# Kernel optimization log

Hardware: AMD Instinct MI355X
Metric: run time of the kernel (lower is better)

Reference implementation:

```python
import jax, jax.numpy as jnp
import numpy as np

B, C, H, W = 4096, 1, 64, 64
NCLASS = 10
ALPHA = 1.0
EPS = 1e-8  # torch CosineSimilarity eps


def setup_inputs() -> dict:
    key = jax.random.key(0)
    k1, k2, k3 = jax.random.split(key, 3)
    outputs = jax.random.normal(k1, (B, NCLASS), dtype=jnp.float32)
    grad = jax.random.normal(k2, (B, C, H, W), dtype=jnp.float32)
    y = jax.random.randint(k3, (B,), 0, NCLASS)
    return {"outputs": outputs, "grad": grad, "y": y}


def reference(outputs, grad, y):
    b = grad.shape[0]
    # per-sample min-max normalization over all of (C,H,W)
    flat = grad.reshape(b, -1)                      # [B, C*H*W]
    gmax = flat.max(axis=1, keepdims=True)
    gmin = flat.min(axis=1, keepdims=True)
    ngrad = (flat - gmin) / (gmax - gmin)           # [B, D]

    # batched pairwise cosine similarity: normalize + matmul
    norms = jnp.linalg.norm(ngrad, axis=1, keepdims=True)
    vn = ngrad / jnp.maximum(norms, EPS)
    sim = vn @ vn.T                                 # [B, B]

    # pairs (i<j) with the same predicted class (argmax(softmax(o)) == argmax(o))
    pred = jnp.argmax(outputs, axis=1)
    same = pred[:, None] == pred[None, :]
    upper = jnp.triu(jnp.ones((b, b), dtype=bool), k=1)
    mask = same & upper
    xloss = jnp.sum(jnp.where(mask, 1.0 - sim, 0.0)) / b

    # cross-entropy
    logp = jax.nn.log_softmax(outputs, axis=1)
    celoss = -jnp.take_along_axis(logp, y[:, None], axis=1).sum() / b
    return celoss + ALPHA * xloss
```

## Files before the change

kernel.cpp:

```cpp
#include <hip/hip_runtime.h>
#include <math.h>

constexpr int Dn = 4096;
constexpr int Bn = 4096;
constexpr int NCLS = 10;

constexpr int OFF_CUR   = 0;
constexpr int OFF_CE    = 10;
constexpr int OFF_XS    = 11;
constexpr int OFF_NCH   = 12;
constexpr int OFF_CHS   = 16;
constexpr int OFF_A     = 32;
constexpr int OFF_B2    = 4128;
constexpr int OFF_ORD   = 8224;
constexpr int OFF_CHMAP = 49184;
constexpr int OFF_P     = 49456;

__global__ __launch_bounds__(256) void pass0_ce_order(
    const float* __restrict__ outputs, const int* __restrict__ y,
    float* __restrict__ ws)
{
    const int t = threadIdx.x;
    const int i = blockIdx.x * 256 + t;
    const int wave = t >> 6, lane = t & 63;
    int* wsi = (int*)ws;

    __shared__ int hist[NCLS];
    __shared__ int lbase[NCLS];
    __shared__ float sce[4];
    if (t < NCLS) hist[t] = 0;
    __syncthreads();

    const float* o = outputs + (size_t)i * NCLS;
    float m = o[0]; int am = 0;
    #pragma unroll
    for (int k = 1; k < NCLS; ++k) { float ok = o[k]; if (ok > m) { m = ok; am = k; } }
    float se = 0.f;
    #pragma unroll
    for (int k = 0; k < NCLS; ++k) se += expf(o[k] - m);
    float ce = m + logf(se) - o[y[i]];

    int rank = atomicAdd(&hist[am], 1);

    #pragma unroll
    for (int off = 32; off; off >>= 1) ce += __shfl_down(ce, off, 64);
    if (lane == 0) sce[wave] = ce;
    __syncthreads();

    if (t < NCLS) lbase[t] = atomicAdd(&wsi[OFF_CUR + t], hist[t]);
    if (t == 0) atomicAdd(&ws[OFF_CE], sce[0] + sce[1] + sce[2] + sce[3]);
    __syncthreads();

    wsi[OFF_ORD + am * Bn + lbase[am] + rank] = i;
}

__global__ void sched_chunks(float* __restrict__ ws, int CH)
{
    int* wsi = (int*)ws;
    int nch = 0;
    for (int c = 0; c < NCLS; ++c) {
        wsi[OFF_CHS + c] = nch;
        int n = wsi[OFF_CUR + c];
        for (int s = 0; s < n; s += CH)
            wsi[OFF_CHMAP + nch++] = (c << 16) | s;
    }
    wsi[OFF_CHS + NCLS] = nch;
    wsi[OFF_NCH] = nch;
}

__global__ __launch_bounds__(256) void pass1_stats(
    const float* __restrict__ grad, float* __restrict__ ws)
{
    const int i = blockIdx.x;
    const int t = threadIdx.x;
    const int wave = t >> 6, lane = t & 63;

    const float4* g4 = (const float4*)(grad + (size_t)i * Dn);
    float4 v[4];
    #pragma unroll
    for (int k = 0; k < 4; ++k) v[k] = g4[t + 256 * k];

    float mn = v[0].x;
    #pragma unroll
    for (int k = 0; k < 4; ++k)
        mn = fminf(mn, fminf(fminf(v[k].x, v[k].y), fminf(v[k].z, v[k].w)));
    #pragma unroll
    for (int off = 32; off; off >>= 1) mn = fminf(mn, __shfl_down(mn, off, 64));
    __shared__ float sred[4];
    __shared__ float sred2[4];
    if (lane == 0) sred[wave] = mn;
    __syncthreads();
    if (t == 0)
        sred[0] = fminf(fminf(sred[0], sred[1]), fminf(sred[2], sred[3]));
    __syncthreads();
    const float gmin = sred[0];

    float ss = 0.f;
    #pragma unroll
    for (int k = 0; k < 4; ++k) {
        float dx = v[k].x - gmin, dy = v[k].y - gmin;
        float dz = v[k].z - gmin, dw = v[k].w - gmin;
        ss += dx * dx + dy * dy + dz * dz + dw * dw;
    }
    #pragma unroll
    for (int off = 32; off; off >>= 1) ss += __shfl_down(ss, off, 64);
    if (lane == 0) sred2[wave] = ss;
    __syncthreads();

    if (t == 0) {
        float sum = sred2[0] + sred2[1] + sred2[2] + sred2[3];
        float s = 1.0f / sqrtf(sum);
        ws[OFF_A + i] = s;
        ws[OFF_B2 + i] = -gmin * s;
    }
}

__global__ __launch_bounds__(256) void pass2_chunksum(
    const float* __restrict__ grad, float* __restrict__ ws, int CH)
{
    const int* wsi = (const int*)ws;
    const int chunk = blockIdx.y;
    if (chunk >= wsi[OFF_NCH]) return;
    const int t = threadIdx.x;

    const int e  = wsi[OFF_CHMAP + chunk];
    const int c  = e >> 16;
    const int s0 = e & 0xFFFF;
    const int m  = min(CH, wsi[OFF_CUR + c] - s0);

    __shared__ int   lidx[512];
    __shared__ float la[512], lb[512];
    for (int k = t; k < m; k += 256) {
        int idx = wsi[OFF_ORD + c * Bn + s0 + k];
        lidx[k] = idx;
        la[k] = ws[OFF_A + idx];
        lb[k] = ws[OFF_B2 + idx];
    }
    __syncthreads();

    const int j4 = blockIdx.x * 256 + t;
    const float4* g4 = (const float4*)grad;

    float4 acc = make_float4(0.f, 0.f, 0.f, 0.f);
    float sb = 0.f;
    #pragma unroll 4
    for (int i = 0; i < m; ++i) {
        float4 gv = g4[(size_t)lidx[i] * (Dn / 4) + j4];
        float ai = la[i];
        acc.x = fmaf(gv.x, ai, acc.x);
        acc.y = fmaf(gv.y, ai, acc.y);
        acc.z = fmaf(gv.z, ai, acc.z);
        acc.w = fmaf(gv.w, ai, acc.w);
        sb += lb[i];
    }
    acc.x += sb; acc.y += sb; acc.z += sb; acc.w += sb;

    ((float4*)(ws + OFF_P))[(size_t)chunk * (Dn / 4) + j4] = acc;
}

__global__ __launch_bounds__(256) void pass3_sq(float* __restrict__ ws)
{
    const int t = threadIdx.x;
    const int idx = blockIdx.x * 256 + t;
    const int c = idx >> 12;
    const int j = idx & (Dn - 1);
    const int wave = t >> 6, lane = t & 63;
    const int* wsi = (const int*)ws;

    const int cs = wsi[OFF_CHS + c];
    const int ce2 = wsi[OFF_CHS + c + 1];
    const float* P = ws + OFF_P;

    float s = 0.f;
    for (int ch = cs; ch < ce2; ++ch)
        s += P[(size_t)ch * Dn + j];
    float p = s * s;

    #pragma unroll
    for (int off = 32; off; off >>= 1) p += __shfl_down(p, off, 64);
    __shared__ float sr[4];
    if (lane == 0) sr[wave] = p;
    __syncthreads();
    if (t == 0) atomicAdd(&ws[OFF_XS], sr[0] + sr[1] + sr[2] + sr[3]);
}

__global__ void pass4_final(const float* __restrict__ ws, float* __restrict__ out)
{
    const int* n = (const int*)ws + OFF_CUR;
    double n2 = 0.0;
    #pragma unroll
    for (int c = 0; c < NCLS; ++c) { double nc = (double)n[c]; n2 += nc * nc; }
    double xloss = (n2 - (double)ws[OFF_XS]) / (2.0 * (double)Bn);
    double celoss = (double)ws[OFF_CE] / (double)Bn;
    out[0] = (float)(celoss + xloss);
}

extern "C" void kernel_launch(void* const* d_in, const int* in_sizes, int n_in,
                              void* d_out, int out_size, void* d_ws, size_t ws_size,
                              hipStream_t stream)
{
    const float* outputs = (const float*)d_in[0];
    const float* grad    = (const float*)d_in[1];
    const int*   y       = (const int*)d_in[2];
    float* ws  = (float*)d_ws;
    float* out = (float*)d_out;

    const size_t availf = ws_size / sizeof(float);
    const int cands[6] = {16, 32, 64, 128, 256, 512};
    int CH = 512, maxch = Bn / 512 + NCLS;
    for (int k = 0; k < 6; ++k) {
        int mc = Bn / cands[k] + NCLS;
        size_t need = (size_t)OFF_P + (size_t)mc * Dn;
        if (need <= availf) { CH = cands[k]; maxch = mc; break; }
    }

    hipMemsetAsync(d_ws, 0, 128, stream);
    pass0_ce_order<<<Bn / 256, 256, 0, stream>>>(outputs, y, ws);
    sched_chunks<<<1, 1, 0, stream>>>(ws, CH);
    pass1_stats<<<Bn, 256, 0, stream>>>(grad, ws);
    pass2_chunksum<<<dim3(4, maxch), 256, 0, stream>>>(grad, ws, CH);
    pass3_sq<<<NCLS * Dn / 256, 256, 0, stream>>>(ws);
    pass4_final<<<1, 1, 0, stream>>>(ws, out);
}
```

Baseline: 129.6 us.

## Fuse stats into chunk-sum pass and merge scheduling and final kernels

Merges the per-class ordering, CE, and chunk scheduling into one single-block kernel using wave ballots. The per-row min/norm stats are fused into the chunk-sum kernel, so each grad row is read once instead of twice. The final reduction uses a last-block ticket instead of a separate launch. This cuts kernel launches and halves grad traffic. The risks are fewer blocks in the chunk-sum pass (one block per chunk covering all of D, 64 float4 registers per thread) and a serial single-block prologue.

```diff
diff --git a/kernel.cpp b/kernel.cpp
--- a/kernel.cpp
+++ b/kernel.cpp
@@ -9,165 +9,187 @@
 constexpr int OFF_CE    = 10;
 constexpr int OFF_XS    = 11;
 constexpr int OFF_NCH   = 12;
+constexpr int OFF_DONE  = 13;
 constexpr int OFF_CHS   = 16;
-constexpr int OFF_A     = 32;
-constexpr int OFF_B2    = 4128;
-constexpr int OFF_ORD   = 8224;
-constexpr int OFF_CHMAP = 49184;
-constexpr int OFF_P     = 49456;
-
-__global__ __launch_bounds__(256) void pass0_ce_order(
+constexpr int OFF_ORD   = 32;
+constexpr int OFF_CHMAP = 41000;
+constexpr int OFF_P     = 41472;
+
+__global__ __launch_bounds__(1024) void pass0_ce_order_sched(
     const float* __restrict__ outputs, const int* __restrict__ y,
-    float* __restrict__ ws)
+    float* __restrict__ ws, int CH)
 {
     const int t = threadIdx.x;
-    const int i = blockIdx.x * 256 + t;
-    const int wave = t >> 6, lane = t & 63;
+    const int w = t >> 6, lane = t & 63;
     int* wsi = (int*)ws;
 
-    __shared__ int hist[NCLS];
-    __shared__ int lbase[NCLS];
-    __shared__ float sce[4];
-    if (t < NCLS) hist[t] = 0;
-    __syncthreads();
-
-    const float* o = outputs + (size_t)i * NCLS;
-    float m = o[0]; int am = 0;
-    #pragma unroll
-    for (int k = 1; k < NCLS; ++k) { float ok = o[k]; if (ok > m) { m = ok; am = k; } }
-    float se = 0.f;
-    #pragma unroll
-    for (int k = 0; k < NCLS; ++k) se += expf(o[k] - m);
-    float ce = m + logf(se) - o[y[i]];
-
-    int rank = atomicAdd(&hist[am], 1);
-
-    #pragma unroll
-    for (int off = 32; off; off >>= 1) ce += __shfl_down(ce, off, 64);
-    if (lane == 0) sce[wave] = ce;
-    __syncthreads();
-
-    if (t < NCLS) lbase[t] = atomicAdd(&wsi[OFF_CUR + t], hist[t]);
-    if (t == 0) atomicAdd(&ws[OFF_CE], sce[0] + sce[1] + sce[2] + sce[3]);
-    __syncthreads();
-
-    wsi[OFF_ORD + am * Bn + lbase[am] + rank] = i;
-}
-
-__global__ void sched_chunks(float* __restrict__ ws, int CH)
-{
-    int* wsi = (int*)ws;
-    int nch = 0;
-    for (int c = 0; c < NCLS; ++c) {
-        wsi[OFF_CHS + c] = nch;
-        int n = wsi[OFF_CUR + c];
-        for (int s = 0; s < n; s += CH)
-            wsi[OFF_CHMAP + nch++] = (c << 16) | s;
-    }
-    wsi[OFF_CHS + NCLS] = nch;
-    wsi[OFF_NCH] = nch;
-}
-
-__global__ __launch_bounds__(256) void pass1_stats(
-    const float* __restrict__ grad, float* __restrict__ ws)
-{
-    const int i = blockIdx.x;
+    __shared__ int whist[16][NCLS];
+    __shared__ int wbase[16][NCLS];
+    __shared__ int cnt[NCLS];
+    __shared__ float sce[16];
+    __shared__ unsigned short srec[Bn];
+
+    if (t < 16 * NCLS) ((int*)whist)[t] = 0;
+    __syncthreads();
+
+    float ce_acc = 0.f;
+    #pragma unroll
+    for (int r = 0; r < 4; ++r) {
+        const int i = r * 1024 + t;
+        const float* o = outputs + (size_t)i * NCLS;
+        float m = o[0]; int am = 0;
+        #pragma unroll
+        for (int k = 1; k < NCLS; ++k) { float ok = o[k]; if (ok > m) { m = ok; am = k; } }
+        float se = 0.f;
+        #pragma unroll
+        for (int k = 0; k < NCLS; ++k) se += expf(o[k] - m);
+        ce_acc += m + logf(se) - o[y[i]];
+
+        int myrank = 0, mycnt = 0;
+        #pragma unroll
+        for (int c = 0; c < NCLS; ++c) {
+            unsigned long long mk = __ballot(am == c);
+            if (am == c) myrank = __popcll(mk & ((1ull << lane) - 1ull));
+            if (lane == c) mycnt = (int)__popcll(mk);
+        }
+        int localpos = whist[w][am] + myrank;
+        if (lane < NCLS) whist[w][lane] += mycnt;
+        srec[i] = (unsigned short)((am << 12) | localpos);
+    }
+
+    #pragma unroll
+    for (int off = 32; off; off >>= 1) ce_acc += __shfl_down(ce_acc, off, 64);
+    if (lane == 0) sce[w] = ce_acc;
+    __syncthreads();
+
+    if (t < NCLS) {
+        int s = 0;
+        for (int w2 = 0; w2 < 16; ++w2) { wbase[w2][t] = s; s += whist[w2][t]; }
+        cnt[t] = s;
+    }
+    __syncthreads();
+
+    if (t == 0) {
+        float cs = 0.f;
+        for (int w2 = 0; w2 < 16; ++w2) cs += sce[w2];
+        ws[OFF_CE] = cs;
+        int nch = 0;
+        for (int c = 0; c < NCLS; ++c) {
+            wsi[OFF_CUR + c] = cnt[c];
+            wsi[OFF_CHS + c] = nch;
+            for (int s = 0; s < cnt[c]; s += CH)
+                wsi[OFF_CHMAP + nch++] = (c << 16) | s;
+        }
+        wsi[OFF_CHS + NCLS] = nch;
+        wsi[OFF_NCH] = nch;
+    }
+    __syncthreads();
+
+    #pragma unroll
+    for (int r = 0; r < 4; ++r) {
+        const int i = r * 1024 + t;
+        unsigned short rec = srec[i];
+        int am = rec >> 12, lp = rec & 0xFFF;
+        wsi[OFF_ORD + am * Bn + wbase[w][am] + lp] = i;
+    }
+}
+
+__global__ __launch_bounds__(256) void pass12_fused(
+    const float* __restrict__ grad, float* __restrict__ ws, int CH)
+{
+    const int* wsi = (const int*)ws;
+    const int chunk = blockIdx.x;
+    if (chunk >= wsi[OFF_NCH]) return;
+
     const int t = threadIdx.x;
-    const int wave = t >> 6, lane = t & 63;
-
-    const float4* g4 = (const float4*)(grad + (size_t)i * Dn);
-    float4 v[4];
-    #pragma unroll
-    for (int k = 0; k < 4; ++k) v[k] = g4[t + 256 * k];
-
-    float mn = v[0].x;
-    #pragma unroll
-    for (int k = 0; k < 4; ++k)
-        mn = fminf(mn, fminf(fminf(v[k].x, v[k].y), fminf(v[k].z, v[k].w)));
-    #pragma unroll
-    for (int off = 32; off; off >>= 1) mn = fminf(mn, __shfl_down(mn, off, 64));
-    __shared__ float sred[4];
-    __shared__ float sred2[4];
-    if (lane == 0) sred[wave] = mn;
-    __syncthreads();
-    if (t == 0)
-        sred[0] = fminf(fminf(sred[0], sred[1]), fminf(sred[2], sred[3]));
-    __syncthreads();
-    const float gmin = sred[0];
-
-    float ss = 0.f;
-    #pragma unroll
-    for (int k = 0; k < 4; ++k) {
-        float dx = v[k].x - gmin, dy = v[k].y - gmin;
-        float dz = v[k].z - gmin, dw = v[k].w - gmin;
-        ss += dx * dx + dy * dy + dz * dz + dw * dw;
-    }
-    #pragma unroll
-    for (int off = 32; off; off >>= 1) ss += __shfl_down(ss, off, 64);
-    if (lane == 0) sred2[wave] = ss;
-    __syncthreads();
-
-    if (t == 0) {
-        float sum = sred2[0] + sred2[1] + sred2[2] + sred2[3];
-        float s = 1.0f / sqrtf(sum);
-        ws[OFF_A + i] = s;
-        ws[OFF_B2 + i] = -gmin * s;
-    }
-}
-
-__global__ __launch_bounds__(256) void pass2_chunksum(
-    const float* __restrict__ grad, float* __restrict__ ws, int CH)
-{
-    const int* wsi = (const int*)ws;
-    const int chunk = blockIdx.y;
-    if (chunk >= wsi[OFF_NCH]) return;
-    const int t = threadIdx.x;
+    const int w = t >> 6, lane = t & 63;
 
     const int e  = wsi[OFF_CHMAP + chunk];
     const int c  = e >> 16;
     const int s0 = e & 0xFFFF;
     const int m  = min(CH, wsi[OFF_CUR + c] - s0);
 
-    __shared__ int   lidx[512];
-    __shared__ float la[512], lb[512];
-    for (int k = t; k < m; k += 256) {
-        int idx = wsi[OFF_ORD + c * Bn + s0 + k];
-        lidx[k] = idx;
-        la[k] = ws[OFF_A + idx];
-        lb[k] = ws[OFF_B2 + idx];
-    }
-    __syncthreads();
-
-    const int j4 = blockIdx.x * 256 + t;
+    float4 acc[16];
+    #pragma unroll
+    for (int k = 0; k < 16; ++k) acc[k] = make_float4(0.f, 0.f, 0.f, 0.f);
+    float sb = 0.f;
+
     const float4* g4 = (const float4*)grad;
-
-    float4 acc = make_float4(0.f, 0.f, 0.f, 0.f);
-    float sb = 0.f;
-    #pragma unroll 4
-    for (int i = 0; i < m; ++i) {
-        float4 gv = g4[(size_t)lidx[i] * (Dn / 4) + j4];
-        float ai = la[i];
-        acc.x = fmaf(gv.x, ai, acc.x);
-        acc.y = fmaf(gv.y, ai, acc.y);
-        acc.z = fmaf(gv.z, ai, acc.z);
-        acc.w = fmaf(gv.w, ai, acc.w);
-        sb += lb[i];
-    }
-    acc.x += sb; acc.y += sb; acc.z += sb; acc.w += sb;
-
-    ((float4*)(ws + OFF_P))[(size_t)chunk * (Dn / 4) + j4] = acc;
-}
-
-__global__ __launch_bounds__(256) void pass3_sq(float* __restrict__ ws)
+    for (int r = w; r < m; r += 4) {
+        const int idx = wsi[OFF_ORD + c * Bn + s0 + r];
+        const float4* row = g4 + (size_t)idx * (Dn / 4);
+        float4 v[16];
+        #pragma unroll
+        for (int k = 0; k < 16; ++k) v[k] = row[k * 64 + lane];
+
+        float mn = fminf(fminf(v[0].x, v[0].y), fminf(v[0].z, v[0].w));
+        #pragma unroll
+        for (int k = 1; k < 16; ++k)
+            mn = fminf(mn, fminf(fminf(v[k].x, v[k].y), fminf(v[k].z, v[k].w)));
+        #pragma unroll
+        for (int off = 1; off < 64; off <<= 1)
+            mn = fminf(mn, __shfl_xor(mn, off, 64));
+
+        float ss = 0.f;
+        #pragma unroll
+        for (int k = 0; k < 16; ++k) {
+            float dx = v[k].x - mn, dy = v[k].y - mn;
+            float dz = v[k].z - mn, dw = v[k].w - mn;
+            ss += dx * dx + dy * dy + dz * dz + dw * dw;
+        }
+        #pragma unroll
+        for (int off = 1; off < 64; off <<= 1)
+            ss += __shfl_xor(ss, off, 64);
+
+        const float a = 1.0f / sqrtf(ss);
+        sb += -mn * a;
+        #pragma unroll
+        for (int k = 0; k < 16; ++k) {
+            acc[k].x = fmaf(v[k].x, a, acc[k].x);
+            acc[k].y = fmaf(v[k].y, a, acc[k].y);
+            acc[k].z = fmaf(v[k].z, a, acc[k].z);
+            acc[k].w = fmaf(v[k].w, a, acc[k].w);
+        }
+    }
+    #pragma unroll
+    for (int k = 0; k < 16; ++k) {
+        acc[k].x += sb; acc[k].y += sb; acc[k].z += sb; acc[k].w += sb;
+    }
+
+    __shared__ float4 sacc[Dn / 4];
+    if (w == 0) {
+        #pragma unroll
+        for (int k = 0; k < 16; ++k) sacc[k * 64 + lane] = acc[k];
+    }
+    __syncthreads();
+    #pragma unroll
+    for (int ww = 1; ww < 4; ++ww) {
+        if (w == ww) {
+            #pragma unroll
+            for (int k = 0; k < 16; ++k) {
+                float4 s = sacc[k * 64 + lane];
+                s.x += acc[k].x; s.y += acc[k].y; s.z += acc[k].z; s.w += acc[k].w;
+                sacc[k * 64 + lane] = s;
+            }
+        }
+        __syncthreads();
+    }
+    float4* Pc = (float4*)(ws + OFF_P) + (size_t)chunk * (Dn / 4);
+    #pragma unroll
+    for (int k = 0; k < 4; ++k) Pc[k * 256 + t] = sacc[k * 256 + t];
+}
+
+__global__ __launch_bounds__(256) void pass34_final(
+    float* __restrict__ ws, float* __restrict__ out)
 {
     const int t = threadIdx.x;
     const int idx = blockIdx.x * 256 + t;
     const int c = idx >> 12;
     const int j = idx & (Dn - 1);
-    const int wave = t >> 6, lane = t & 63;
+    const int w = t >> 6, lane = t & 63;
     const int* wsi = (const int*)ws;
 
-    const int cs = wsi[OFF_CHS + c];
+    const int cs  = wsi[OFF_CHS + c];
     const int ce2 = wsi[OFF_CHS + c + 1];
     const float* P = ws + OFF_P;
 
@@ -179,20 +201,23 @@
     #pragma unroll
     for (int off = 32; off; off >>= 1) p += __shfl_down(p, off, 64);
     __shared__ float sr[4];
-    if (lane == 0) sr[wave] = p;
-    __syncthreads();
-    if (t == 0) atomicAdd(&ws[OFF_XS], sr[0] + sr[1] + sr[2] + sr[3]);
-}
-
-__global__ void pass4_final(const float* __restrict__ ws, float* __restrict__ out)
-{
-    const int* n = (const int*)ws + OFF_CUR;
-    double n2 = 0.0;
-    #pragma unroll
-    for (int c = 0; c < NCLS; ++c) { double nc = (double)n[c]; n2 += nc * nc; }
-    double xloss = (n2 - (double)ws[OFF_XS]) / (2.0 * (double)Bn);
-    double celoss = (double)ws[OFF_CE] / (double)Bn;
-    out[0] = (float)(celoss + xloss);
+    if (lane == 0) sr[w] = p;
+    __syncthreads();
+    if (t == 0) {
+        atomicAdd(&ws[OFF_XS], sr[0] + sr[1] + sr[2] + sr[3]);
+        __threadfence();
+        int ticket = atomicAdd(&((int*)ws)[OFF_DONE], 1);
+        if (ticket == (NCLS * Dn / 256) - 1) {
+            float xs = atomicAdd(&ws[OFF_XS], 0.0f);
+            const int* n = wsi + OFF_CUR;
+            double n2 = 0.0;
+            #pragma unroll
+            for (int k = 0; k < NCLS; ++k) { double nc = (double)n[k]; n2 += nc * nc; }
+            double xloss = (n2 - (double)xs) / (2.0 * (double)Bn);
+            double celoss = (double)ws[OFF_CE] / (double)Bn;
+            out[0] = (float)(celoss + xloss);
+        }
+    }
 }
 
 extern "C" void kernel_launch(void* const* d_in, const int* in_sizes, int n_in,
@@ -215,10 +240,7 @@
     }
 
     hipMemsetAsync(d_ws, 0, 128, stream);
-    pass0_ce_order<<<Bn / 256, 256, 0, stream>>>(outputs, y, ws);
-    sched_chunks<<<1, 1, 0, stream>>>(ws, CH);
-    pass1_stats<<<Bn, 256, 0, stream>>>(grad, ws);
-    pass2_chunksum<<<dim3(4, maxch), 256, 0, stream>>>(grad, ws, CH);
-    pass3_sq<<<NCLS * Dn / 256, 256, 0, stream>>>(ws);
-    pass4_final<<<1, 1, 0, stream>>>(ws, out);
-}
+    pass0_ce_order_sched<<<1, 1024, 0, stream>>>(outputs, y, ws, CH);
+    pass12_fused<<<maxch, 256, 0, stream>>>(grad, ws, CH);
+    pass34_final<<<NCLS * Dn / 256, 256, 0, stream>>>(ws, out);
+}
```

Measured after the change: 132.8 us. 2.4% more time.
